# Kernel tuning notes

Measured on AMD Instinct MI355X. Metric: run time of the kernel, lower is better.

The kernel has to match this reference:

```python
import jax, jax.numpy as jnp
import numpy as np

B, N, DEG = 8, 8192, 16
E = B * N * DEG
K1 = 2458  # ceil(0.3*8192)
K2 = 738   # ceil(0.3*2458)
NUM_CLASSES = 10


def gat(x, src, dst, emask, W, a_s, a_d, bias):
    # PyG GATConv with add_self_loops=True, negative_slope=0.2, concat heads
    n = x.shape[0]
    H, F = a_s.shape
    xp = (x @ W).reshape(n, H, F)                      # [n,H,F]
    al_s = (xp * a_s).sum(-1)                          # [n,H]
    al_d = (xp * a_d).sum(-1)
    loops = jnp.arange(n, dtype=src.dtype)
    s2 = jnp.concatenate([src, loops])
    d2 = jnp.concatenate([dst, loops])
    m2 = jnp.concatenate([emask, jnp.ones(n, bool)])
    e = jax.nn.leaky_relu(al_s[s2] + al_d[d2], 0.2)    # [E+n,H]
    e = jnp.where(m2[:, None], e, -1e9)
    emax = jax.ops.segment_max(e, d2, num_segments=n)
    ex = jnp.where(m2[:, None], jnp.exp(e - emax[d2]), 0.0)
    den = jax.ops.segment_sum(ex, d2, num_segments=n)
    msg = ex[:, :, None] * xp[s2]                      # [E+n,H,F]
    out = jax.ops.segment_sum(msg, d2, num_segments=n) / den[:, :, None]
    return out.reshape(n, H * F) + bias


def inorm(x):
    # PyG InstanceNorm (affine=False): per-graph per-channel normalization
    xb = x.reshape(B, -1, x.shape[-1])
    mu = xb.mean(1, keepdims=True)
    var = ((xb - mu) ** 2).mean(1, keepdims=True)
    return ((xb - mu) / jnp.sqrt(var + 1e-5)).reshape(x.shape)


def topk_pool(x, src, dst, emask, p, k):
    # TopKPooling: score = tanh(x.p/|p|), keep top-k per graph, scale x by score
    n_tot = x.shape[0]
    n = n_tot // B
    score = jnp.tanh((x @ p) / jnp.linalg.norm(p))
    sv, si = jax.lax.top_k(score.reshape(B, n), k)     # [B,k]
    xg = jnp.take_along_axis(x.reshape(B, n, -1), si[:, :, None], axis=1)
    xnew = (xg * sv[:, :, None]).reshape(B * k, -1)
    perm = (si + (jnp.arange(B) * n)[:, None]).reshape(-1)
    newid = jnp.full(n_tot, -1, dtype=src.dtype).at[perm].set(
        jnp.arange(B * k, dtype=src.dtype))
    ns, nd = newid[src], newid[dst]
    m = emask & (ns >= 0) & (nd >= 0)
    return xnew, jnp.maximum(ns, 0), jnp.maximum(nd, 0), m


def setup_inputs() -> dict:
    key = jax.random.key(0)
    ks = jax.random.split(key, 32)
    pos = jax.random.normal(ks[0], (B * N, 3), jnp.float32)
    offs = jnp.repeat(jnp.arange(B, dtype=jnp.int32) * N, N * DEG)
    src = jax.random.randint(ks[1], (E,), 0, N, jnp.int32) + offs
    dst = jax.random.randint(ks[2], (E,), 0, N, jnp.int32) + offs

    def lin(k, fi, fo):
        return jax.random.normal(k, (fi, fo), jnp.float32) * (1.0 / np.sqrt(fi))

    d = dict(pos=pos, src=src, dst=dst)
    d['W1'] = lin(ks[3], 3, 32);   d['a_s1'] = jax.random.normal(ks[4], (2, 16)) * 0.2
    d['a_d1'] = jax.random.normal(ks[5], (2, 16)) * 0.2
    d['b1'] = jnp.zeros((32,));    d['p1'] = jax.random.normal(ks[6], (32,))
    d['W2'] = lin(ks[7], 32, 128); d['a_s2'] = jax.random.normal(ks[8], (2, 64)) * 0.2
    d['a_d2'] = jax.random.normal(ks[9], (2, 64)) * 0.2
    d['b2'] = jnp.zeros((128,));   d['p2'] = jax.random.normal(ks[10], (128,))
    d['W3'] = lin(ks[11], 128, 256); d['a_s3'] = jax.random.normal(ks[12], (1, 256)) * 0.1
    d['a_d3'] = jax.random.normal(ks[13], (1, 256)) * 0.1
    d['b3'] = jnp.zeros((256,))
    d['gw1'] = lin(ks[14], 256, 64);  d['gb1'] = jnp.zeros((64,))
    d['gw2'] = lin(ks[15], 64, 1);    d['gb2'] = jnp.zeros((1,))
    d['aw'] = lin(ks[16], 256, 256);  d['ab'] = jnp.zeros((256,))
    d['w1'] = lin(ks[17], 256, 512);  d['bb1'] = jnp.zeros((512,))
    d['w2'] = lin(ks[18], 512, 128);  d['bb2'] = jnp.zeros((128,))
    d['w3'] = lin(ks[19], 128, NUM_CLASSES); d['bb3'] = jnp.zeros((NUM_CLASSES,))
    return d


def reference(pos, src, dst, W1, a_s1, a_d1, b1, p1, W2, a_s2, a_d2, b2, p2,
              W3, a_s3, a_d3, b3, gw1, gb1, gw2, gb2, aw, ab,
              w1, bb1, w2, bb2, w3, bb3):
    emask = jnp.ones(src.shape[0], bool)
    x = gat(pos, src, dst, emask, W1, a_s1, a_d1, b1)
    x = jax.nn.elu(inorm(x))
    x, src, dst, emask = topk_pool(x, src, dst, emask, p1, K1)
    x = gat(x, src, dst, emask, W2, a_s2, a_d2, b2)
    x = jax.nn.elu(inorm(x))
    x, src, dst, emask = topk_pool(x, src, dst, emask, p2, K2)
    x = gat(x, src, dst, emask, W3, a_s3, a_d3, b3)
    x = jax.nn.elu(inorm(x))
    # GlobalAttention: gate_nn = Linear(256,64)+ELU+Linear(64,1); nn = Linear+ELU
    gate = jax.nn.elu(x @ gw1 + gb1) @ gw2 + gb2       # [M,1]
    h = jax.nn.elu(x @ aw + ab)                        # [M,256]
    a = jax.nn.softmax(gate.reshape(B, K2, 1), axis=1)
    g = (a * h.reshape(B, K2, 256)).sum(1)             # [B,256]
    z = jax.nn.elu(g @ w1 + bb1)   # dropout inactive in eval
    z = jax.nn.elu(z @ w2 + bb2)
    z = z @ w3 + bb3
    return jax.nn.log_softmax(z, axis=1)
```

## Files before the change

### kernel.cpp

```cpp
#include <hip/hip_runtime.h>
#include <cstdint>
#include <cstddef>

#define DI __device__ __forceinline__

namespace pk {

constexpr int NB1 = 65536;
constexpr int NE  = 1048576;
constexpr int BG  = 8;
constexpr int NPG1 = 8192;
constexpr int EPG1 = NE/BG;
constexpr int KP1 = 2458;
constexpr int KP2 = 738;
constexpr int NN2 = BG*KP1;
constexpr int NN3 = BG*KP2;
constexpr int REG2 = 16384;
constexpr int REG3 = 4096;
constexpr int CAP2 = BG*REG2;
constexpr int CAP3 = BG*REG3;
constexpr int CPB1 = 8;

DI float lrelu(float x){ return x > 0.f ? x : 0.2f*x; }
DI float eluf(float x){ return x > 0.f ? x : expf(x) - 1.f; }

DI int swz_block(){
  int nb = gridDim.x, b = blockIdx.x;
  if((nb & 7) == 0) return (b & 7)*(nb >> 3) + (b >> 3);
  return b;
}

__global__ __launch_bounds__(1024) void k_s1_front(
    const float* __restrict__ pos, const float* __restrict__ W,
    const float* __restrict__ as_, const float* __restrict__ ad_,
    float* __restrict__ xp, float* __restrict__ als, float* __restrict__ ald,
    const int* __restrict__ de, int* __restrict__ part){
  __shared__ int h[NPG1];
  int tid = threadIdx.x;
  if(blockIdx.x < 64){
    int i = blockIdx.x*1024 + tid;
    float p0=pos[3*i], p1=pos[3*i+1], p2=pos[3*i+2];
    float row[32];
#pragma unroll
    for(int c=0;c<32;c++) row[c] = p0*W[c] + p1*W[32+c] + p2*W[64+c];
    float s0=0.f,d0=0.f,s1=0.f,d1=0.f;
#pragma unroll
    for(int f=0;f<16;f++){
      s0 += row[f]*as_[f];        d0 += row[f]*ad_[f];
      s1 += row[16+f]*as_[16+f];  d1 += row[16+f]*ad_[16+f];
    }
    float4* o = reinterpret_cast<float4*>(xp + (size_t)i*32);
#pragma unroll
    for(int q=0;q<8;q++) o[q] = make_float4(row[4*q],row[4*q+1],row[4*q+2],row[4*q+3]);
    als[2*i]=s0; als[2*i+1]=s1; ald[2*i]=d0; ald[2*i+1]=d1;
    return;
  }
  int bb = blockIdx.x - 64;
  int g = bb >> 3, t = bb & 7;
  for(int i=tid;i<NPG1;i+=1024) h[i]=0;
  __syncthreads();
  const int4* de4 = (const int4*)(de + g*EPG1 + t*(EPG1/CPB1));
  int lo = g*NPG1;
  int4 d0 = de4[0*1024+tid], d1 = de4[1*1024+tid];
  int4 d2 = de4[2*1024+tid], d3 = de4[3*1024+tid];
  atomicAdd(&h[d0.x-lo],1); atomicAdd(&h[d0.y-lo],1);
  atomicAdd(&h[d0.z-lo],1); atomicAdd(&h[d0.w-lo],1);
  atomicAdd(&h[d1.x-lo],1); atomicAdd(&h[d1.y-lo],1);
  atomicAdd(&h[d1.z-lo],1); atomicAdd(&h[d1.w-lo],1);
  atomicAdd(&h[d2.x-lo],1); atomicAdd(&h[d2.y-lo],1);
  atomicAdd(&h[d2.z-lo],1); atomicAdd(&h[d2.w-lo],1);
  atomicAdd(&h[d3.x-lo],1); atomicAdd(&h[d3.y-lo],1);
  atomicAdd(&h[d3.z-lo],1); atomicAdd(&h[d3.w-lo],1);
  __syncthreads();
  int* pp = part + (size_t)(g*CPB1+t)*NPG1;
  for(int i=tid;i<NPG1;i+=1024) pp[i]=h[i];
}

__global__ __launch_bounds__(1024) void k_scan1(
    const int* __restrict__ part, int* __restrict__ cnt,
    int* __restrict__ rowptr){
  __shared__ int wsum[16];
  int g = blockIdx.x;
  int tid = threadIdx.x, lane = tid & 63, w = tid >> 6;
  constexpr int PER = NPG1/1024;
  int base = g*NPG1;
  int i0 = tid*PER;
  int v[PER]; int s = 0;
#pragma unroll
  for(int j=0;j<PER;j++){
    int i = i0+j;
    int x = 0;
#pragma unroll
    for(int p=0;p<CPB1;p++) x += part[(size_t)(g*CPB1+p)*NPG1 + i];
    cnt[base+i] = x;
    v[j] = s; s += x;
  }
  int inc = s;
  for(int o=1;o<64;o<<=1){ int t2=__shfl_up(inc,o,64); if(lane>=o) inc+=t2; }
  if(lane==63) wsum[w]=inc;
  __syncthreads();
  int wb=0;
  for(int k=0;k<w;k++) wb+=wsum[k];
  int tb = g*EPG1 + wb + inc - s;
#pragma unroll
  for(int j=0;j<PER;j++) rowptr[base+i0+j] = tb + v[j];
}

__global__ __launch_bounds__(1024) void k_tile_scatter(
    const int* __restrict__ se, const int* __restrict__ de,
    const int* __restrict__ rowptr, int* __restrict__ eo){
  __shared__ int cur[256];
  int tid = threadIdx.x;
  int g = blockIdx.x & 7, t = blockIdx.x >> 3;
  int lo = g*NPG1 + t*256;
  if(tid < 256) cur[tid] = rowptr[lo + tid];
  __syncthreads();
  const int4* de4 = (const int4*)(de + g*EPG1);
  const int4* se4 = (const int4*)(se + g*EPG1);
  for(int it=0; it<4; it++){
    int4 bd[8], bs[8];
#pragma unroll
    for(int j=0;j<8;j++){
      int idx = (it*8+j)*1024 + tid;
      bd[j] = de4[idx]; bs[j] = se4[idx];
    }
#pragma unroll
    for(int j=0;j<8;j++){
      int4 d = bd[j], s = bs[j];
      int d0=d.x-lo; if((unsigned)d0<256u){ int p=atomicAdd(&cur[d0],1); eo[p]=s.x; }
      int d1=d.y-lo; if((unsigned)d1<256u){ int p=atomicAdd(&cur[d1],1); eo[p]=s.y; }
      int d2=d.z-lo; if((unsigned)d2<256u){ int p=atomicAdd(&cur[d2],1); eo[p]=s.z; }
      int d3=d.w-lo; if((unsigned)d3<256u){ int p=atomicAdd(&cur[d3],1); eo[p]=s.w; }
    }
  }
}

__global__ __launch_bounds__(256) void k_scatter_r(
    const int* __restrict__ se, const int* __restrict__ de,
    const int* __restrict__ gcnt, int reg,
    int* __restrict__ cursor, int* __restrict__ eo){
  int i = swz_block()*256 + threadIdx.x;
  int g = i / reg, loc = i % reg;
  if(loc < gcnt[g]){
    int p = atomicAdd(&cursor[de[i]], 1);
    eo[p] = se[i];
  }
}

__global__ __launch_bounds__(256) void k_edge_compact(
    const int* __restrict__ se, const int* __restrict__ de,
    const int* __restrict__ gcnt_in, int fixed_in, int bpg, int reg_in,
    const int* __restrict__ newid, int* __restrict__ gcnt_out,
    int* __restrict__ ons, int* __restrict__ ond, int reg_out,
    int* __restrict__ cnt){
  __shared__ int s_a[4096];
  __shared__ int s_b[4096];
  __shared__ int run, tbase;
  int tid = threadIdx.x;
  if(tid == 0) run = 0;
  __syncthreads();
  int blk = swz_block();
  int g = blk / bpg, t = blk % bpg;
  int mg = gcnt_in ? gcnt_in[g] : fixed_in;
  if(mg > reg_in) mg = reg_in;
  int base_l = t*4096;
  if(base_l < mg){
    const int* deb = de + (size_t)g*reg_in + base_l;
    const int* seb = se + (size_t)g*reg_in + base_l;
    const int4* de4 = (const int4*)deb;
    const int4* se4 = (const int4*)seb;
    int4 BD[4], BS[4];
#pragma unroll
    for(int j=0;j<4;j++){ BD[j]=de4[j*256+tid]; BS[j]=se4[j*256+tid]; }
    int cl = 0;
#pragma unroll
    for(int j=0;j<4;j++){
      int eb = base_l + (j*256+tid)*4;
      int dd[4]={BD[j].x,BD[j].y,BD[j].z,BD[j].w};
      int ss[4]={BS[j].x,BS[j].y,BS[j].z,BS[j].w};
#pragma unroll
      for(int q=0;q<4;q++){
        if(eb+q < mg){
          int a = newid[ss[q]], b = newid[dd[q]];
          if(a>=0 && b>=0){ cl++; atomicAdd(&cnt[b], 1); }
        }
      }
    }
    int p0 = 0;
    if(cl) p0 = atomicAdd(&run, cl);
#pragma unroll
    for(int j=0;j<4;j++){
      int eb = base_l + (j*256+tid)*4;
      int dd[4]={BD[j].x,BD[j].y,BD[j].z,BD[j].w};
      int ss[4]={BS[j].x,BS[j].y,BS[j].z,BS[j].w};
#pragma unroll
      for(int q=0;q<4;q++){
        if(eb+q < mg){
          int a = newid[ss[q]], b = newid[dd[q]];
          if(a>=0 && b>=0){ s_a[p0]=a; s_b[p0]=b; p0++; }
        }
      }
    }
  }
  __syncthreads();
  int ns = run;
  if(tid==0) tbase = ns ? atomicAdd(&gcnt_out[g], ns) : 0;
  __syncthreads();
  int tb = tbase;
  for(int j=tid; j<ns; j+=256){
    int s2 = tb + j;
    if(s2 < reg_out){ ons[(size_t)g*reg_out+s2]=s_a[j]; ond[(size_t)g*reg_out+s2]=s_b[j]; }
  }
}

template<int PER>
DI void scan256(const int* __restrict__ cnt, int R, int estride,
                int* __restrict__ rowptr, int* __restrict__ cursor, int g){
  __shared__ int wsum[4];
  int tid = threadIdx.x, lane = tid & 63, w = tid >> 6;
  int base = g*R;
  int i0 = tid*PER;
  int v[PER]; int s = 0;
#pragma unroll
  for(int j=0;j<PER;j++){ int i=i0+j; int x=(i<R)?cnt[base+i]:0; v[j]=s; s+=x; }
  int inc = s;
  for(int o=1;o<64;o<<=1){ int t=__shfl_up(inc,o,64); if(lane>=o) inc+=t; }
  if(lane==63) wsum[w]=inc;
  __syncthreads();
  int wb=0;
  for(int k=0;k<w;k++) wb+=wsum[k];
  int tb = g*estride + wb + inc - s;
#pragma unroll
  for(int j=0;j<PER;j++){
    int i=i0+j;
    if(i<R){
      int e=tb+v[j];
      rowptr[base+i]=e;
      cursor[base+i]=e;
    }
  }
}

template<int H,int F,int EB>
__global__ __launch_bounds__(256) void k_gat_fused(
    const float* __restrict__ xp, const float* __restrict__ als,
    const float* __restrict__ ald, const int* __restrict__ rowptr,
    const int* __restrict__ cnt, const int* __restrict__ esrc,
    const float* __restrict__ bias, float* __restrict__ out,
    float* __restrict__ accum, int RPG, int bpg){
  constexpr int C = H*F, C4 = C/4;
  constexpr int NPB = 256/C4;
  __shared__ float psum[4][C], psq[4][C];
  int tid = threadIdx.x;
  int nl = tid / C4, p = tid % C4;
  int work = (blockIdx.x & 7)*(gridDim.x >> 3) + (blockIdx.x >> 3);
  int g = work / bpg, t = work - g*bpg;
  int loc = t*NPB + nl;
  int node = g*RPG + loc;
  int hh = (4*p)/F;
  const float4* xp4 = (const float4*)xp;
  float4 r = make_float4(0.f,0.f,0.f,0.f);
  bool valid = loc < RPG;
  if(valid){
    float dvh = ald[node*H+hh];
    float sw  = expf(lrelu(als[node*H+hh] + dvh));
    float4 xs = xp4[(size_t)node*C4 + p];
    float den = sw;
    float ax=sw*xs.x, ay=sw*xs.y, az=sw*xs.z, aw_=sw*xs.w;
    int r0  = rowptr[node];
    int deg = cnt[node];
    for(int j=0; j<deg; j+=EB){
      int idx[EB]; float wv[EB]; float4 v[EB];
#pragma unroll
      for(int q=0;q<EB;q++)
        idx[q] = (j+q < deg) ? esrc[r0+j+q] : node;
#pragma unroll
      for(int q=0;q<EB;q++)
        wv[q] = als[idx[q]*H+hh];
#pragma unroll
      for(int q=0;q<EB;q++)
        v[q] = xp4[(size_t)idx[q]*C4 + p];
#pragma unroll
      for(int q=0;q<EB;q++){
        float w = (j+q < deg) ? expf(lrelu(wv[q] + dvh)) : 0.f;
        den += w;
        ax += w*v[q].x; ay += w*v[q].y; az += w*v[q].z; aw_ += w*v[q].w;
      }
    }
    float inv = 1.f / den;
    float4 bv = ((const float4*)bias)[p];
    r.x=ax*inv+bv.x; r.y=ay*inv+bv.y; r.z=az*inv+bv.z; r.w=aw_*inv+bv.w;
    ((float4*)out)[(size_t)node*C4 + p] = r;
  }
  float sx=r.x, sy=r.y, sz=r.z, sw2=r.w;
  float qx=r.x*r.x, qy=r.y*r.y, qz=r.z*r.z, qw=r.w*r.w;
#pragma unroll
  for(int off=C4; off<64; off<<=1){
    sx += __shfl_down(sx, off, 64); sy += __shfl_down(sy, off, 64);
    sz += __shfl_down(sz, off, 64); sw2 += __shfl_down(sw2, off, 64);
    qx += __shfl_down(qx, off, 64); qy += __shfl_down(qy, off, 64);
    qz += __shfl_down(qz, off, 64); qw += __shfl_down(qw, off, 64);
  }
  int lane = tid & 63, w = tid >> 6;
  if(lane < C4){
    psum[w][4*lane+0]=sx; psum[w][4*lane+1]=sy;
    psum[w][4*lane+2]=sz; psum[w][4*lane+3]=sw2;
    psq[w][4*lane+0]=qx;  psq[w][4*lane+1]=qy;
    psq[w][4*lane+2]=qz;  psq[w][4*lane+3]=qw;
  }
  __syncthreads();
  if(tid < C){
    float ts = psum[0][tid]+psum[1][tid]+psum[2][tid]+psum[3][tid];
    float tq = psq[0][tid]+psq[1][tid]+psq[2][tid]+psq[3][tid];
    atomicAdd(&accum[(g*C+tid)*2],   ts);
    atomicAdd(&accum[(g*C+tid)*2+1], tq);
  }
}

template<int K,int CO,int NPG,int H,int PER>
__global__ __launch_bounds__(256) void k_gemm_al(
    const float* __restrict__ X, const int* __restrict__ oldid,
    const float* __restrict__ scale, const float* __restrict__ W,
    float* __restrict__ Y, const float* __restrict__ a_s,
    const float* __restrict__ a_d, float* __restrict__ als,
    float* __restrict__ ald, int n, int ngemm,
    const int* __restrict__ scnt, int sR, int sstride,
    int* __restrict__ srowptr, int* __restrict__ scursor){
  constexpr int SUB = 256/CO;
  constexpr int NB = SUB*NPG;
  __shared__ float xs[NB][K];
  __shared__ float ps[4][NPG], pd[4][NPG];
  if((int)blockIdx.x >= ngemm){
    scan256<PER>(scnt, sR, sstride, srowptr, scursor, (int)blockIdx.x - ngemm);
    return;
  }
  int tid = threadIdx.x;
  int c = tid % CO, sg = tid / CO;
  int n0 = blockIdx.x * NB;
  for(int idx=tid; idx<NB*K; idx+=256){
    int r = idx / K, k = idx % K;
    int row = n0 + r;
    float v = 0.f;
    if(row < n){
      int orow = oldid[row];
      v = X[(size_t)orow*K + k] * scale[row];
    }
    xs[r][k] = v;
  }
  __syncthreads();
  float acc[NPG];
#pragma unroll
  for(int q=0;q<NPG;q++) acc[q]=0.f;
  for(int k=0;k<K;k++){
    float wv = W[(size_t)k*CO + c];
#pragma unroll
    for(int q=0;q<NPG;q++) acc[q] += xs[sg*NPG+q][k]*wv;
  }
  float asc = a_s[c], adc = a_d[c];
  float vs[NPG], vd[NPG];
#pragma unroll
  for(int q=0;q<NPG;q++){
    int row = n0 + sg*NPG + q;
    if(row < n) Y[(size_t)row*CO + c] = acc[q];
    vs[q] = acc[q]*asc; vd[q] = acc[q]*adc;
  }
#pragma unroll
  for(int o=32;o>0;o>>=1){
#pragma unroll
    for(int q=0;q<NPG;q++){
      vs[q] += __shfl_down(vs[q], o, 64);
      vd[q] += __shfl_down(vd[q], o, 64);
    }
  }
  int lane = tid & 63, w = tid >> 6;
  if(H == 2){
    if(lane == 0){
      int sg_ = w >> 1, h = w & 1;
#pragma unroll
      for(int q=0;q<NPG;q++){
        int row = n0 + sg_*NPG + q;
        if(row < n){ als[row*2+h] = vs[q]; ald[row*2+h] = vd[q]; }
      }
    }
  } else {
    if(lane == 0){
#pragma unroll
      for(int q=0;q<NPG;q++){ ps[w][q]=vs[q]; pd[w][q]=vd[q]; }
    }
    __syncthreads();
    if(tid < NPG){
      float s=0.f, d=0.f;
      for(int ww=0;ww<4;ww++){ s+=ps[ww][tid]; d+=pd[ww][tid]; }
      int row = n0 + tid;
      if(row < n){ als[row]=s; ald[row]=d; }
    }
  }
}

DI float inorm_of(const float* accum, int gc, float R, float x){
  float s = accum[gc*2], sq = accum[gc*2+1];
  float mu = s / R;
  float var = fmaxf(sq/R - mu*mu, 0.f);
  return eluf((x-mu)*rsqrtf(var+1e-5f));
}

template<int C>
__global__ __launch_bounds__(256) void k_inorm_score(
    float* __restrict__ x, const float* __restrict__ accum,
    const float* __restrict__ p, int R, int total,
    float* __restrict__ score, unsigned* __restrict__ u){
  __shared__ float rvp[256], rpp[256];
  int tid = threadIdx.x;
  int i = blockIdx.x*256 + tid;
  int c = tid & (C-1);
  bool act = i < total;
  float v = 0.f, pv = 0.f;
  if(act){
    int g = i / (R*C);
    v = inorm_of(accum, g*C+c, (float)R, x[i]);
    x[i] = v;
    pv = p[c];
  }
  rvp[tid] = v*pv; rpp[tid] = pv*pv;
  __syncthreads();
#pragma unroll
  for(int s2=C/2; s2>0; s2>>=1){
    if(c < s2){ rvp[tid]+=rvp[tid+s2]; rpp[tid]+=rpp[tid+s2]; }
    __syncthreads();
  }
  if(act && c==0){
    float sv = tanhf(rvp[tid]*rsqrtf(rpp[tid]));
    int row = i / C;
    score[row] = sv;
    unsigned bts = __float_as_uint(sv);
    u[row] = (bts & 0x80000000u) ? ~bts : (bts | 0x80000000u);
  }
}

__global__ __launch_bounds__(1024) void k_topk(
    const unsigned* __restrict__ u, const float* __restrict__ score,
    int R, int Ksel, int* __restrict__ newid, int* __restrict__ oldid,
    float* __restrict__ scale){
  __shared__ int hist[2048];
  __shared__ int seg[32];
  __shared__ int sh_b, sh_k;
  __shared__ int wsA[16], wsB[16];
  __shared__ int carr0, carr1;
  int g = blockIdx.x, tid = threadIdx.x, lane = tid&63, w = tid>>6;
  const unsigned* ug = u + (size_t)g*R;
  unsigned prefix = 0;
  int K = Ksel;
  for(int lev=0; lev<3; lev++){
    int shf = (lev==0)?21:((lev==1)?10:0);
    int nb  = (lev==2)?1024:2048;
    for(int i=tid;i<2048;i+=1024) hist[i]=0;
    __syncthreads();
    for(int i=tid;i<R;i+=1024){
      unsigned v = ug[i];
      bool ok = (lev==0) || (lev==1 && (v>>21)==prefix) || (lev==2 && (v>>10)==prefix);
      if(ok) atomicAdd(&hist[(v>>shf)&(nb-1)], 1);
    }
    __syncthreads();
    int W = nb/32;
    if(tid<32){ int s=0; int lo=nb-W*(tid+1); for(int b=lo;b<lo+W;b++) s+=hist[b]; seg[tid]=s; }
    __syncthreads();
    if(tid==0){
      int kk=K, sgi=0;
      while(seg[sgi]<kk){ kk-=seg[sgi]; sgi++; }
      int b = nb-1-W*sgi;
      while(hist[b]<kk){ kk-=hist[b]; b--; }
      sh_b=b; sh_k=kk;
    }
    __syncthreads();
    int b = sh_b; K = sh_k;
    if(lev==0) prefix = (unsigned)b;
    else if(lev==1) prefix = (prefix<<11) | (unsigned)b;
    else prefix = (prefix<<10) | (unsigned)b;
    __syncthreads();
  }
  unsigned thr = prefix;
  int need = K;
  if(tid==0){ carr0=0; carr1=0; }
  __syncthreads();
  for(int bb=0; bb<R; bb+=1024){
    int i = bb + tid; bool in = i < R;
    unsigned uv = in ? ug[i] : 0u;
    int eq = (in && uv==thr) ? 1:0;
    int gt = (in && uv>thr) ? 1:0;
    int inc = eq;
    for(int o=1;o<64;o<<=1){ int t=__shfl_up(inc,o,64); if(lane>=o) inc+=t; }
    if(lane==63) wsA[w]=inc;
    __syncthreads();
    int wb=0; for(int k=0;k<w;k++) wb+=wsA[k];
    int eq_excl = carr0 + wb + inc - eq;
    int take = (gt || (eq && eq_excl<need)) ? 1 : 0;
    int inc2 = take;
    for(int o=1;o<64;o<<=1){ int t=__shfl_up(inc2,o,64); if(lane>=o) inc2+=t; }
    if(lane==63) wsB[w]=inc2;
    __syncthreads();
    int wb2=0; for(int k=0;k<w;k++) wb2+=wsB[k];
    int pos = carr1 + wb2 + inc2 - take;
    if(take){
      int nr = g*Ksel + pos;
      newid[(size_t)g*R+i] = nr;
      oldid[nr] = g*R+i;
      scale[nr] = score[(size_t)g*R+i];
    }
    __syncthreads();
    if(tid==1023){ carr0 += wb + inc; carr1 += wb2 + inc2; }
    __syncthreads();
  }
}

__global__ __launch_bounds__(256) void k_gate_fused(
    const float* __restrict__ X, const float* __restrict__ accum,
    const float* __restrict__ gw1, const float* __restrict__ gb1,
    const float* __restrict__ gw2, const float* __restrict__ gb2,
    float* __restrict__ gatev, int n){
  __shared__ float xs[8][256];
  int tid = threadIdx.x;
  int n0 = blockIdx.x*8;
  for(int idx=tid; idx<2048; idx+=256){
    int r = idx >> 8, k = idx & 255;
    int row = n0 + r;
    float v = 0.f;
    if(row < n){
      int g = row / KP2;
      v = inorm_of(accum, g*256+k, (float)KP2, X[(size_t)row*256 + k]);
    }
    xs[r][k] = v;
  }
  __syncthreads();
  int sg = tid >> 6, c = tid & 63;
  float a0 = 0.f, a1 = 0.f;
#pragma unroll 8
  for(int k=0;k<256;k++){
    float w = gw1[k*64+c];
    a0 = fmaf(xs[sg][k],   w, a0);
    a1 = fmaf(xs[sg+4][k], w, a1);
  }
  float gb = gb1[c], g2 = gw2[c];
  float v0 = eluf(a0 + gb) * g2;
  float v1 = eluf(a1 + gb) * g2;
#pragma unroll
  for(int o=32;o>0;o>>=1){
    v0 += __shfl_down(v0, o, 64);
    v1 += __shfl_down(v1, o, 64);
  }
  if(c==0){
    int r0 = n0 + sg, r1 = n0 + sg + 4;
    if(r0 < n) gatev[r0] = v0 + gb2[0];
    if(r1 < n) gatev[r1] = v1 + gb2[0];
  }
}

__global__ __launch_bounds__(256) void k_attn_gemm(
    const float* __restrict__ X, const float* __restrict__ accum,
    const float* __restrict__ W, const float* __restrict__ bias,
    const float* __restrict__ gatev, float* __restrict__ gvec){
  __shared__ float xs[8][256];
  __shared__ float red[256];
  int tid = threadIdx.x;
  int t = blockIdx.x, g = blockIdx.y;
  int r0 = t*8;
  float mx = -1e30f;
  for(int r=tid;r<KP2;r+=256) mx = fmaxf(mx, gatev[g*KP2+r]);
  red[tid]=mx; __syncthreads();
  for(int s=128;s>0;s>>=1){ if(tid<s) red[tid]=fmaxf(red[tid],red[tid+s]); __syncthreads(); }
  mx = red[0]; __syncthreads();
  float sm=0.f;
  for(int r=tid;r<KP2;r+=256) sm += expf(gatev[g*KP2+r]-mx);
  red[tid]=sm; __syncthreads();
  for(int s=128;s>0;s>>=1){ if(tid<s) red[tid]+=red[tid+s]; __syncthreads(); }
  float inv = 1.f/red[0];
  __syncthreads();
  for(int idx=tid; idx<2048; idx+=256){
    int r = idx >> 8, k = idx & 255;
    int lr = r0 + r;
    float v = 0.f;
    if(lr < KP2){
      int row = g*KP2 + lr;
      v = inorm_of(accum, g*256+k, (float)KP2, X[(size_t)row*256 + k]);
    }
    xs[r][k] = v;
  }
  __syncthreads();
  int c = tid;
  float acc[8];
#pragma unroll
  for(int q=0;q<8;q++) acc[q]=0.f;
  for(int k=0;k<256;k++){
    float wv = W[(size_t)k*256 + c];
#pragma unroll
    for(int q=0;q<8;q++) acc[q] += xs[q][k]*wv;
  }
  float bv = bias[c];
  float tot = 0.f;
#pragma unroll
  for(int q=0;q<8;q++){
    int lr = r0 + q;
    if(lr < KP2){
      float h = eluf(acc[q] + bv);
      tot += expf(gatev[g*KP2+lr]-mx) * h;
    }
  }
  atomicAdd(&gvec[g*256+c], tot*inv);
}

template<int K,int CO,int ACT>
__global__ __launch_bounds__(256) void k_mlp_t(
    const float* __restrict__ X, const float* __restrict__ W,
    const float* __restrict__ b, float* __restrict__ Y, int n){
  int i = blockIdx.x*256+threadIdx.x;
  if(i>=n*CO) return;
  int r=i/CO, c=i%CO;
  const float* xr = X + (size_t)r*K;
  float a=0.f;
#pragma unroll 16
  for(int k=0;k<K;k++) a = fmaf(xr[k], W[(size_t)k*CO+c], a);
  a += b[c];
  if(ACT) a = eluf(a);
  Y[i]=a;
}

__global__ __launch_bounds__(64) void k_head(
    const float* __restrict__ z2, const float* __restrict__ w3,
    const float* __restrict__ b3, float* __restrict__ out){
  __shared__ float zc[10]; __shared__ float mred, sred;
  int g=blockIdx.x, tid=threadIdx.x;
  if(tid<10){
    float a=0.f;
#pragma unroll 16
    for(int k=0;k<128;k++) a += z2[g*128+k]*w3[k*10+tid];
    zc[tid]=a+b3[tid];
  }
  __syncthreads();
  if(tid==0){
    float m=zc[0];
    for(int k=1;k<10;k++) m=fmaxf(m,zc[k]);
    float s=0.f;
    for(int k=0;k<10;k++) s+=expf(zc[k]-m);
    mred=m; sred=logf(s);
  }
  __syncthreads();
  if(tid<10) out[g*10+tid]=zc[tid]-mred-sred;
}

}

extern "C" void kernel_launch(void* const* d_in, const int* in_sizes, int n_in,
                              void* d_out, int out_size, void* d_ws, size_t ws_size,
                              hipStream_t stream){
  using namespace pk;
  (void)in_sizes; (void)n_in; (void)out_size;
  const float* pos = (const float*)d_in[0];
  const int*   src = (const int*)d_in[1];
  const int*   dst = (const int*)d_in[2];
  const float* W1  = (const float*)d_in[3];
  const float* as1 = (const float*)d_in[4];
  const float* ad1 = (const float*)d_in[5];
  const float* b1  = (const float*)d_in[6];
  const float* p1  = (const float*)d_in[7];
  const float* W2  = (const float*)d_in[8];
  const float* as2 = (const float*)d_in[9];
  const float* ad2 = (const float*)d_in[10];
  const float* b2  = (const float*)d_in[11];
  const float* p2  = (const float*)d_in[12];
  const float* W3  = (const float*)d_in[13];
  const float* as3 = (const float*)d_in[14];
  const float* ad3 = (const float*)d_in[15];
  const float* b3  = (const float*)d_in[16];
  const float* gw1 = (const float*)d_in[17];
  const float* gb1 = (const float*)d_in[18];
  const float* gw2 = (const float*)d_in[19];
  const float* gb2 = (const float*)d_in[20];
  const float* aw  = (const float*)d_in[21];
  const float* ab  = (const float*)d_in[22];
  const float* w1  = (const float*)d_in[23];
  const float* bb1 = (const float*)d_in[24];
  const float* w2  = (const float*)d_in[25];
  const float* bb2 = (const float*)d_in[26];
  const float* w3  = (const float*)d_in[27];
  const float* bb3 = (const float*)d_in[28];
  float* out = (float*)d_out;

  char* base = (char*)d_ws; size_t off = 0;
  auto alloc = [&](size_t nbytes)->char*{
    char* p = base + off; off = (off + nbytes + 255) & ~(size_t)255; return p;
  };
  int*   cnt2  = (int*)alloc((size_t)NN2*4);
  int*   cnt3  = (int*)alloc((size_t)NN3*4);
  int*   ecnt2 = (int*)alloc((size_t)BG*4);
  int*   ecnt3 = (int*)alloc((size_t)BG*4);
  float* acc1  = (float*)alloc((size_t)BG*32*2*4);
  float* acc2  = (float*)alloc((size_t)BG*128*2*4);
  float* acc3  = (float*)alloc((size_t)BG*256*2*4);
  float* gvec  = (float*)alloc((size_t)BG*256*4);
  size_t zend = off;
  int*   newid1 = (int*)alloc((size_t)NB1*4);
  int*   newid2 = (int*)alloc((size_t)NN2*4);
  size_t fstart = (size_t)((char*)newid1 - base);
  size_t fend = off;
  int*      part1  = (int*)alloc((size_t)BG*CPB1*NPG1*4);
  int*      cnt1   = (int*)alloc((size_t)NB1*4);
  float*    xp1    = (float*)alloc((size_t)NB1*32*4);
  float*    als1   = (float*)alloc((size_t)NB1*2*4);
  float*    ald1   = (float*)alloc((size_t)NB1*2*4);
  int*      rowptr1= (int*)alloc((size_t)NB1*4);
  int*      esrc1  = (int*)alloc((size_t)NE*4);
  float*    out1   = (float*)alloc((size_t)NB1*32*4);
  float*    score1 = (float*)alloc((size_t)NB1*4);
  unsigned* u1     = (unsigned*)alloc((size_t)NB1*4);
  int*      oldid1 = (int*)alloc((size_t)NN2*4);
  float*    scale1 = (float*)alloc((size_t)NN2*4);
  int*      ns2    = (int*)alloc((size_t)CAP2*4);
  int*      nd2    = (int*)alloc((size_t)CAP2*4);
  int*      rowptr2= (int*)alloc((size_t)NN2*4);
  int*      cursor2= (int*)alloc((size_t)NN2*4);
  int*      esrc2  = (int*)alloc((size_t)CAP2*4);
  float*    xp2    = (float*)alloc((size_t)NN2*128*4);
  float*    als2   = (float*)alloc((size_t)NN2*2*4);
  float*    ald2   = (float*)alloc((size_t)NN2*2*4);
  float*    out2   = (float*)alloc((size_t)NN2*128*4);
  float*    score2 = (float*)alloc((size_t)NN2*4);
  unsigned* u2     = (unsigned*)alloc((size_t)NN2*4);
  int*      oldid2 = (int*)alloc((size_t)NN3*4);
  float*    scale2 = (float*)alloc((size_t)NN3*4);
  int*      ns3    = (int*)alloc((size_t)CAP3*4);
  int*      nd3    = (int*)alloc((size_t)CAP3*4);
  int*      rowptr3= (int*)alloc((size_t)NN3*4);
  int*      cursor3= (int*)alloc((size_t)NN3*4);
  int*      esrc3  = (int*)alloc((size_t)CAP3*4);
  float*    xp3    = (float*)alloc((size_t)NN3*256*4);
  float*    als3   = (float*)alloc((size_t)NN3*4);
  float*    ald3   = (float*)alloc((size_t)NN3*4);
  float*    out3   = (float*)alloc((size_t)NN3*256*4);
  float*    gatev  = (float*)alloc((size_t)NN3*4);
  float*    z1     = (float*)alloc((size_t)BG*512*4);
  float*    z2     = (float*)alloc((size_t)BG*128*4);
  if(off > ws_size) return;

  auto cdiv = [](int a, int b){ return (a+b-1)/b; };

  hipMemsetAsync(base, 0, zend, stream);
  hipMemsetAsync(base + fstart, 0xFF, fend - fstart, stream);

  k_s1_front<<<128,1024,0,stream>>>(pos,W1,as1,ad1,xp1,als1,ald1,dst,part1);
  k_scan1<<<BG,1024,0,stream>>>(part1,cnt1,rowptr1);
  k_tile_scatter<<<256,1024,0,stream>>>(src,dst,rowptr1,esrc1);
  k_gat_fused<2,16,16><<<2048,256,0,stream>>>(xp1,als1,ald1,rowptr1,cnt1,esrc1,b1,out1,acc1,NPG1,256);
  k_inorm_score<32><<<cdiv(NB1*32,256),256,0,stream>>>(out1,acc1,p1,8192,NB1*32,score1,u1);
  k_topk<<<BG,1024,0,stream>>>(u1,score1,8192,KP1,newid1,oldid1,scale1);
  k_edge_compact<<<BG*32,256,0,stream>>>(src,dst,nullptr,EPG1,32,EPG1,newid1,ecnt2,ns2,nd2,REG2,cnt2);
  {
    int ngemm = cdiv(NN2,8);
    k_gemm_al<32,128,4,2,10><<<ngemm+BG,256,0,stream>>>(
        out1,oldid1,scale1,W2,xp2,as2,ad2,als2,ald2,NN2,
        ngemm,cnt2,KP1,REG2,rowptr2,cursor2);
  }
  k_scatter_r<<<CAP2/256,256,0,stream>>>(ns2,nd2,ecnt2,REG2,cursor2,esrc2);
  k_gat_fused<2,64,8><<<8*308,256,0,stream>>>(xp2,als2,ald2,rowptr2,cnt2,esrc2,b2,out2,acc2,KP1,308);
  k_inorm_score<128><<<cdiv(NN2*128,256),256,0,stream>>>(out2,acc2,p2,KP1,NN2*128,score2,u2);
  k_topk<<<BG,1024,0,stream>>>(u2,score2,KP1,KP2,newid2,oldid2,scale2);
  k_edge_compact<<<BG*4,256,0,stream>>>(ns2,nd2,ecnt2,0,4,REG2,newid2,ecnt3,ns3,nd3,REG3,cnt3);
  {
    int ngemm = cdiv(NN3,4);
    k_gemm_al<128,256,4,1,3><<<ngemm+BG,256,0,stream>>>(
        out2,oldid2,scale2,W3,xp3,as3,ad3,als3,ald3,NN3,
        ngemm,cnt3,KP2,REG3,rowptr3,cursor3);
  }
  k_scatter_r<<<CAP3/256,256,0,stream>>>(ns3,nd3,ecnt3,REG3,cursor3,esrc3);
  k_gat_fused<1,256,4><<<8*185,256,0,stream>>>(xp3,als3,ald3,rowptr3,cnt3,esrc3,b3,out3,acc3,KP2,185);
  k_gate_fused<<<cdiv(NN3,8),256,0,stream>>>(out3,acc3,gw1,gb1,gw2,gb2,gatev,NN3);
  k_attn_gemm<<<dim3(cdiv(KP2,8),BG),256,0,stream>>>(out3,acc3,aw,ab,gatev,gvec);
  k_mlp_t<256,512,1><<<cdiv(BG*512,256),256,0,stream>>>(gvec,w1,bb1,z1,BG);
  k_mlp_t<512,128,1><<<cdiv(BG*128,256),256,0,stream>>>(z1,w2,bb2,z2,BG);
  k_head<<<BG,64,0,stream>>>(z2,w3,bb3,out);
}
```

Baseline: 420.3 us.

## Pre-bucket stage-1 edges by destination tile and defer instance-norm write-back

The histogram kernel now also bins each edge into a per-graph, per-256-node tile bucket as a packed src/dst word. The scatter kernel then reads only its own bucket instead of scanning all edges of the graph 32 times. Separately, the inorm+score kernel no longer writes normalized activations back; the gather in the next GEMM recomputes inorm+ELU on the fly for the selected rows only. This adds a bucket buffer and global atomics, and bucket capacity BKT=5120 assumes at most that many edges per tile.

```diff
diff --git a/kernel.cpp b/kernel.cpp
--- a/kernel.cpp
+++ b/kernel.cpp
@@ -20,6 +20,8 @@
 constexpr int CAP2 = BG*REG2;
 constexpr int CAP3 = BG*REG3;
 constexpr int CPB1 = 8;
+constexpr int NTILE = 32;
+constexpr int BKT = 5120;
 
 DI float lrelu(float x){ return x > 0.f ? x : 0.2f*x; }
 DI float eluf(float x){ return x > 0.f ? x : expf(x) - 1.f; }
@@ -34,8 +36,11 @@
     const float* __restrict__ pos, const float* __restrict__ W,
     const float* __restrict__ as_, const float* __restrict__ ad_,
     float* __restrict__ xp, float* __restrict__ als, float* __restrict__ ald,
-    const int* __restrict__ de, int* __restrict__ part){
+    const int* __restrict__ se, const int* __restrict__ de,
+    int* __restrict__ part, int* __restrict__ bcur, int* __restrict__ bpk){
   __shared__ int h[NPG1];
+  __shared__ int hbase[NTILE];
+  __shared__ int hc[NTILE];
   int tid = threadIdx.x;
   if(blockIdx.x < 64){
     int i = blockIdx.x*1024 + tid;
@@ -56,24 +61,39 @@
     return;
   }
   int bb = blockIdx.x - 64;
-  int g = bb >> 3, t = bb & 7;
+  int g = bb & 7, t = bb >> 3;
   for(int i=tid;i<NPG1;i+=1024) h[i]=0;
   __syncthreads();
   const int4* de4 = (const int4*)(de + g*EPG1 + t*(EPG1/CPB1));
+  const int4* se4 = (const int4*)(se + g*EPG1 + t*(EPG1/CPB1));
   int lo = g*NPG1;
-  int4 d0 = de4[0*1024+tid], d1 = de4[1*1024+tid];
-  int4 d2 = de4[2*1024+tid], d3 = de4[3*1024+tid];
-  atomicAdd(&h[d0.x-lo],1); atomicAdd(&h[d0.y-lo],1);
-  atomicAdd(&h[d0.z-lo],1); atomicAdd(&h[d0.w-lo],1);
-  atomicAdd(&h[d1.x-lo],1); atomicAdd(&h[d1.y-lo],1);
-  atomicAdd(&h[d1.z-lo],1); atomicAdd(&h[d1.w-lo],1);
-  atomicAdd(&h[d2.x-lo],1); atomicAdd(&h[d2.y-lo],1);
-  atomicAdd(&h[d2.z-lo],1); atomicAdd(&h[d2.w-lo],1);
-  atomicAdd(&h[d3.x-lo],1); atomicAdd(&h[d3.y-lo],1);
-  atomicAdd(&h[d3.z-lo],1); atomicAdd(&h[d3.w-lo],1);
-  __syncthreads();
+  int4 dv[4], sv[4];
+#pragma unroll
+  for(int j=0;j<4;j++){ dv[j]=de4[j*1024+tid]; sv[j]=se4[j*1024+tid]; }
+  int dl[16], sl[16];
+#pragma unroll
+  for(int j=0;j<4;j++){
+    dl[4*j+0]=dv[j].x-lo; dl[4*j+1]=dv[j].y-lo; dl[4*j+2]=dv[j].z-lo; dl[4*j+3]=dv[j].w-lo;
+    sl[4*j+0]=sv[j].x-lo; sl[4*j+1]=sv[j].y-lo; sl[4*j+2]=sv[j].z-lo; sl[4*j+3]=sv[j].w-lo;
+  }
+#pragma unroll
+  for(int q=0;q<16;q++) atomicAdd(&h[dl[q]],1);
+  __syncthreads();
+  if(tid < NTILE){
+    int ssum = 0;
+    for(int i=0;i<256;i++) ssum += h[tid*256+i];
+    hbase[tid] = atomicAdd(&bcur[g*NTILE+tid], ssum);
+    hc[tid] = 0;
+  }
   int* pp = part + (size_t)(g*CPB1+t)*NPG1;
   for(int i=tid;i<NPG1;i+=1024) pp[i]=h[i];
+  __syncthreads();
+#pragma unroll
+  for(int q=0;q<16;q++){
+    int tt = dl[q] >> 8;
+    int p = atomicAdd(&hc[tt],1) + hbase[tt];
+    bpk[(size_t)(g*NTILE+tt)*BKT + p] = (sl[q]<<13) | dl[q];
+  }
 }
 
 __global__ __launch_bounds__(1024) void k_scan1(
@@ -106,8 +126,8 @@
   for(int j=0;j<PER;j++) rowptr[base+i0+j] = tb + v[j];
 }
 
-__global__ __launch_bounds__(1024) void k_tile_scatter(
-    const int* __restrict__ se, const int* __restrict__ de,
+__global__ __launch_bounds__(1024) void k_scatter_b(
+    const int* __restrict__ bcur, const int* __restrict__ bpk,
     const int* __restrict__ rowptr, int* __restrict__ eo){
   __shared__ int cur[256];
   int tid = threadIdx.x;
@@ -115,23 +135,14 @@
   int lo = g*NPG1 + t*256;
   if(tid < 256) cur[tid] = rowptr[lo + tid];
   __syncthreads();
-  const int4* de4 = (const int4*)(de + g*EPG1);
-  const int4* se4 = (const int4*)(se + g*EPG1);
-  for(int it=0; it<4; it++){
-    int4 bd[8], bs[8];
-#pragma unroll
-    for(int j=0;j<8;j++){
-      int idx = (it*8+j)*1024 + tid;
-      bd[j] = de4[idx]; bs[j] = se4[idx];
-    }
-#pragma unroll
-    for(int j=0;j<8;j++){
-      int4 d = bd[j], s = bs[j];
-      int d0=d.x-lo; if((unsigned)d0<256u){ int p=atomicAdd(&cur[d0],1); eo[p]=s.x; }
-      int d1=d.y-lo; if((unsigned)d1<256u){ int p=atomicAdd(&cur[d1],1); eo[p]=s.y; }
-      int d2=d.z-lo; if((unsigned)d2<256u){ int p=atomicAdd(&cur[d2],1); eo[p]=s.z; }
-      int d3=d.w-lo; if((unsigned)d3<256u){ int p=atomicAdd(&cur[d3],1); eo[p]=s.w; }
-    }
+  int cnt = bcur[g*NTILE + t];
+  const int* bp = bpk + (size_t)(g*NTILE + t)*BKT;
+  for(int i=tid; i<cnt; i+=1024){
+    int pk = bp[i];
+    int dlo = pk & 8191;
+    int slo = pk >> 13;
+    int p = atomicAdd(&cur[dlo - t*256], 1);
+    eo[p] = g*NPG1 + slo;
   }
 }
 
@@ -317,9 +328,17 @@
   }
 }
 
+DI float inorm_of(const float* accum, int gc, float R, float x){
+  float s = accum[gc*2], sq = accum[gc*2+1];
+  float mu = s / R;
+  float var = fmaxf(sq/R - mu*mu, 0.f);
+  return eluf((x-mu)*rsqrtf(var+1e-5f));
+}
+
 template<int K,int CO,int NPG,int H,int PER>
 __global__ __launch_bounds__(256) void k_gemm_al(
-    const float* __restrict__ X, const int* __restrict__ oldid,
+    const float* __restrict__ X, const float* __restrict__ naccum, int nRPG,
+    const int* __restrict__ oldid,
     const float* __restrict__ scale, const float* __restrict__ W,
     float* __restrict__ Y, const float* __restrict__ a_s,
     const float* __restrict__ a_d, float* __restrict__ als,
@@ -343,7 +362,8 @@
     float v = 0.f;
     if(row < n){
       int orow = oldid[row];
-      v = X[(size_t)orow*K + k] * scale[row];
+      int og = orow / nRPG;
+      v = inorm_of(naccum, og*K + k, (float)nRPG, X[(size_t)orow*K + k]) * scale[row];
     }
     xs[r][k] = v;
   }
@@ -397,16 +417,9 @@
   }
 }
 
-DI float inorm_of(const float* accum, int gc, float R, float x){
-  float s = accum[gc*2], sq = accum[gc*2+1];
-  float mu = s / R;
-  float var = fmaxf(sq/R - mu*mu, 0.f);
-  return eluf((x-mu)*rsqrtf(var+1e-5f));
-}
-
 template<int C>
 __global__ __launch_bounds__(256) void k_inorm_score(
-    float* __restrict__ x, const float* __restrict__ accum,
+    const float* __restrict__ x, const float* __restrict__ accum,
     const float* __restrict__ p, int R, int total,
     float* __restrict__ score, unsigned* __restrict__ u){
   __shared__ float rvp[256], rpp[256];
@@ -418,7 +431,6 @@
   if(act){
     int g = i / (R*C);
     v = inorm_of(accum, g*C+c, (float)R, x[i]);
-    x[i] = v;
     pv = p[c];
   }
   rvp[tid] = v*pv; rpp[tid] = pv*pv;
@@ -696,6 +708,7 @@
   float* acc2  = (float*)alloc((size_t)BG*128*2*4);
   float* acc3  = (float*)alloc((size_t)BG*256*2*4);
   float* gvec  = (float*)alloc((size_t)BG*256*4);
+  int*   bcur1 = (int*)alloc((size_t)BG*NTILE*4);
   size_t zend = off;
   int*   newid1 = (int*)alloc((size_t)NB1*4);
   int*   newid2 = (int*)alloc((size_t)NN2*4);
@@ -703,6 +716,7 @@
   size_t fend = off;
   int*      part1  = (int*)alloc((size_t)BG*CPB1*NPG1*4);
   int*      cnt1   = (int*)alloc((size_t)NB1*4);
+  int*      bpk1   = (int*)alloc((size_t)BG*NTILE*BKT*4);
   float*    xp1    = (float*)alloc((size_t)NB1*32*4);
   float*    als1   = (float*)alloc((size_t)NB1*2*4);
   float*    ald1   = (float*)alloc((size_t)NB1*2*4);
@@ -745,9 +759,9 @@
   hipMemsetAsync(base, 0, zend, stream);
   hipMemsetAsync(base + fstart, 0xFF, fend - fstart, stream);
 
-  k_s1_front<<<128,1024,0,stream>>>(pos,W1,as1,ad1,xp1,als1,ald1,dst,part1);
+  k_s1_front<<<128,1024,0,stream>>>(pos,W1,as1,ad1,xp1,als1,ald1,src,dst,part1,bcur1,bpk1);
   k_scan1<<<BG,1024,0,stream>>>(part1,cnt1,rowptr1);
-  k_tile_scatter<<<256,1024,0,stream>>>(src,dst,rowptr1,esrc1);
+  k_scatter_b<<<256,1024,0,stream>>>(bcur1,bpk1,rowptr1,esrc1);
   k_gat_fused<2,16,16><<<2048,256,0,stream>>>(xp1,als1,ald1,rowptr1,cnt1,esrc1,b1,out1,acc1,NPG1,256);
   k_inorm_score<32><<<cdiv(NB1*32,256),256,0,stream>>>(out1,acc1,p1,8192,NB1*32,score1,u1);
   k_topk<<<BG,1024,0,stream>>>(u1,score1,8192,KP1,newid1,oldid1,scale1);
@@ -755,7 +769,7 @@
   {
     int ngemm = cdiv(NN2,8);
     k_gemm_al<32,128,4,2,10><<<ngemm+BG,256,0,stream>>>(
-        out1,oldid1,scale1,W2,xp2,as2,ad2,als2,ald2,NN2,
+        out1,acc1,NPG1,oldid1,scale1,W2,xp2,as2,ad2,als2,ald2,NN2,
         ngemm,cnt2,KP1,REG2,rowptr2,cursor2);
   }
   k_scatter_r<<<CAP2/256,256,0,stream>>>(ns2,nd2,ecnt2,REG2,cursor2,esrc2);
@@ -766,7 +780,7 @@
   {
     int ngemm = cdiv(NN3,4);
     k_gemm_al<128,256,4,1,3><<<ngemm+BG,256,0,stream>>>(
-        out2,oldid2,scale2,W3,xp3,as3,ad3,als3,ald3,NN3,
+        out2,acc2,KP1,oldid2,scale2,W3,xp3,as3,ad3,als3,ald3,NN3,
         ngemm,cnt3,KP2,REG3,rowptr3,cursor3);
   }
   k_scatter_r<<<CAP3/256,256,0,stream>>>(ns3,nd3,ecnt3,REG3,cursor3,esrc3);
```

New measurement: 408.6 us. 1.03x faster.
